# Performance work log

Hardware: AMD Instinct MI355X
Metric: run time of the kernel (lower is better)

## Reference

```python
import jax, jax.numpy as jnp
import numpy as np
import math

D_MODEL, H, D_FF = 1024, 16, 4096
B, S = 4, 2048
EPS = 1e-6

def layer_norm(x, alpha, beta):
    # Faithful to torch: x.std uses Bessel correction (ddof=1), eps added to std.
    mean = jnp.mean(x, axis=-1, keepdims=True)
    std = jnp.std(x, axis=-1, keepdims=True, ddof=1)
    return alpha * (x - mean) / (std + EPS) + beta

def setup_inputs() -> dict:
    key = jax.random.key(0)
    ks = jax.random.split(key, 8)
    sc = 0.02
    return {
        "x": jax.random.normal(ks[0], (B, S, D_MODEL), jnp.float32),
        "mask": jnp.ones((B, 1, 1, S), jnp.int32),
        "wq": jax.random.normal(ks[1], (D_MODEL, D_MODEL), jnp.float32) * sc,
        "wk": jax.random.normal(ks[2], (D_MODEL, D_MODEL), jnp.float32) * sc,
        "wv": jax.random.normal(ks[3], (D_MODEL, D_MODEL), jnp.float32) * sc,
        "wo": jax.random.normal(ks[4], (D_MODEL, D_MODEL), jnp.float32) * sc,
        "w1": jax.random.normal(ks[5], (D_MODEL, D_FF), jnp.float32) * sc,
        "b1": jnp.zeros((D_FF,), jnp.float32),
        "w2": jax.random.normal(ks[6], (D_FF, D_MODEL), jnp.float32) * sc,
        "b2": jnp.zeros((D_MODEL,), jnp.float32),
        "ln1_a": jnp.ones((D_MODEL,), jnp.float32),
        "ln1_b": jnp.zeros((D_MODEL,), jnp.float32),
        "ln2_a": jnp.ones((D_MODEL,), jnp.float32),
        "ln2_b": jnp.zeros((D_MODEL,), jnp.float32),
    }

def mha(xn, mask, wq, wk, wv, wo):
    b, s, d = xn.shape
    d_k = d // H
    q = (xn @ wq).reshape(b, s, H, d_k).transpose(0, 2, 1, 3)  # [B,H,S,dk]
    k = (xn @ wk).reshape(b, s, H, d_k).transpose(0, 2, 1, 3)
    v = (xn @ wv).reshape(b, s, H, d_k).transpose(0, 2, 1, 3)
    scores = jnp.einsum('bhqd,bhkd->bhqk', q, k) / math.sqrt(d_k)
    scores = jnp.where(mask == 0, -1e9, scores)
    attn = jax.nn.softmax(scores, axis=-1)
    out = jnp.einsum('bhqk,bhkd->bhqd', attn, v)
    out = out.transpose(0, 2, 1, 3).reshape(b, s, d)
    return out @ wo

def reference(x, mask, wq, wk, wv, wo, w1, b1, w2, b2, ln1_a, ln1_b, ln2_a, ln2_b):
    # Pre-LN residual 1: self-attention (dropout=0 / eval mode -> identity)
    xn = layer_norm(x, ln1_a, ln1_b)
    x = x + mha(xn, mask, wq, wk, wv, wo)
    # Pre-LN residual 2: FFN
    xn = layer_norm(x, ln2_a, ln2_b)
    ff = jax.nn.relu(xn @ w1 + b1) @ w2 + b2
    return x + ff
```

## Files before the change

kernel.cpp:

```cpp
#include <hip/hip_runtime.h>
#include <hip/hip_bf16.h>

typedef __bf16 bf16x8 __attribute__((ext_vector_type(8)));
typedef __bf16 bf16x4 __attribute__((ext_vector_type(4)));
typedef float  f32x4  __attribute__((ext_vector_type(4)));

#define MFMA(a, b, c) __builtin_amdgcn_mfma_f32_16x16x32_bf16((a), (b), (c), 0, 0, 0)

#define GLOAD16(gp, lp) __builtin_amdgcn_global_load_lds(                      \
    (const __attribute__((address_space(1))) void*)(gp),                       \
    (__attribute__((address_space(3))) void*)(lp), 16, 0, 0)

__device__ inline unsigned int pkbf(float a, float b) {
    __bf16 x = (__bf16)a, y = (__bf16)b;
    return (unsigned int)*(unsigned short*)&x |
           ((unsigned int)*(unsigned short*)&y << 16);
}

__global__ __launch_bounds__(256) void transpose_cvt(
    const float* __restrict__ src, __bf16* __restrict__ dst, int Kd, int Nd)
{
    __shared__ float tile[32][33];
    const int k0 = blockIdx.y * 32, n0 = blockIdx.x * 32;
    const int t = threadIdx.x;
    const int r = t >> 5, c = t & 31;
#pragma unroll
    for (int i = 0; i < 4; ++i)
        tile[r + i * 8][c] = src[(long)(k0 + r + i * 8) * Nd + n0 + c];
    __syncthreads();
#pragma unroll
    for (int i = 0; i < 4; ++i)
        dst[(long)(n0 + r + i * 8) * Kd + k0 + c] = (__bf16)tile[c][r + i * 8];
}

__global__ __launch_bounds__(256) void transpose_v(
    const __bf16* __restrict__ V, __bf16* __restrict__ Vt)
{
    __shared__ __bf16 tile[32][33];
    const int bh = blockIdx.z;
    const int s0 = blockIdx.x * 32, d0 = blockIdx.y * 32;
    const int t = threadIdx.x, r = t >> 5, c = t & 31;
    const __bf16* Vp = V + (long)bh * 2048 * 64;
    __bf16* Tp = Vt + (long)bh * 64 * 2048;
#pragma unroll
    for (int i = 0; i < 4; ++i)
        tile[r + i * 8][c] = Vp[(long)(s0 + r + i * 8) * 64 + d0 + c];
    __syncthreads();
#pragma unroll
    for (int i = 0; i < 4; ++i)
        Tp[(long)(d0 + r + i * 8) * 2048 + s0 + c] = tile[c][r + i * 8];
}

__global__ __launch_bounds__(256) void ln_kernel(
    const float* __restrict__ in, const float* __restrict__ ga,
    const float* __restrict__ gb, __bf16* __restrict__ out)
{
    const int row = blockIdx.x;
    const int t = threadIdx.x;
    const float4 xv = *(const float4*)(in + (long)row * 1024 + t * 4);
    float s  = xv.x + xv.y + xv.z + xv.w;
    float sq = xv.x * xv.x + xv.y * xv.y + xv.z * xv.z + xv.w * xv.w;
#pragma unroll
    for (int off = 32; off; off >>= 1) {
        s  += __shfl_xor(s, off);
        sq += __shfl_xor(sq, off);
    }
    __shared__ float red[8];
    const int w = t >> 6;
    if ((t & 63) == 0) { red[w * 2] = s; red[w * 2 + 1] = sq; }
    __syncthreads();
    s  = red[0] + red[2] + red[4] + red[6];
    sq = red[1] + red[3] + red[5] + red[7];
    const float mean = s * (1.0f / 1024.0f);
    const float var  = fmaxf((sq - s * mean) * (1.0f / 1023.0f), 0.0f);
    const float dinv = 1.0f / (sqrtf(var) + 1e-6f);
    const float4 av = *(const float4*)(ga + t * 4);
    const float4 bv = *(const float4*)(gb + t * 4);
    bf16x4 o;
    o[0] = (__bf16)((xv.x - mean) * dinv * av.x + bv.x);
    o[1] = (__bf16)((xv.y - mean) * dinv * av.y + bv.y);
    o[2] = (__bf16)((xv.z - mean) * dinv * av.z + bv.z);
    o[3] = (__bf16)((xv.w - mean) * dinv * av.w + bv.w);
    *(bf16x4*)(out + (long)row * 1024 + t * 4) = o;
}

template <int MODE>
__global__ __launch_bounds__(256) void gemm_bt(
    const __bf16* __restrict__ A, const __bf16* __restrict__ Bt,
    int M, int N, int K,
    const float* __restrict__ bias, const float* resid,
    float* outf, __bf16* __restrict__ outb,
    __bf16* __restrict__ qb, __bf16* __restrict__ kb, __bf16* __restrict__ vb)
{
    __shared__ __align__(16) __bf16 Alds[128 * 32];
    __shared__ __align__(16) __bf16 Blds[128 * 32];

    const int t = threadIdx.x;
    const int lane = t & 63, w = t >> 6;
    const int wr = w >> 1, wc = w & 1;
    const int g = lane >> 4, l15 = lane & 15;

    const int nwg = gridDim.x * gridDim.y;
    const int hwid = blockIdx.y * gridDim.x + blockIdx.x;
    const int wid = (hwid & 7) * (nwg >> 3) + (hwid >> 3);
    const int bm = (wid / gridDim.x) * 128;
    const int bn = (wid % gridDim.x) * 128;

    const int cr = t >> 2;
    const int cc = (t & 3) * 8;
    const __bf16* Ag  = A  + (long)(bm + cr) * K + cc;
    const __bf16* Ag2 = Ag + (long)64 * K;
    const __bf16* Bg  = Bt + (long)(bn + cr) * K + cc;
    const __bf16* Bg2 = Bg + (long)64 * K;
    char* Alp = (char*)Alds + t * 16;
    char* Blp = (char*)Blds + t * 16;

    f32x4 acc[4][4] = {};
    const int nk = K / 32;

    for (int kt = 0; kt < nk; ++kt) {
        const long ko = (long)kt * 32;
        __syncthreads();
        GLOAD16(Ag + ko,  Alp);
        GLOAD16(Ag2 + ko, Alp + 4096);
        GLOAD16(Bg + ko,  Blp);
        GLOAD16(Bg2 + ko, Blp + 4096);
        __syncthreads();
        bf16x8 af[4], bfr[4];
#pragma unroll
        for (int mi = 0; mi < 4; ++mi)
            af[mi] = *(const bf16x8*)(Alds + (wr * 64 + mi * 16 + l15) * 32 + g * 8);
#pragma unroll
        for (int ni = 0; ni < 4; ++ni)
            bfr[ni] = *(const bf16x8*)(Blds + (wc * 64 + ni * 16 + l15) * 32 + g * 8);
#pragma unroll
        for (int mi = 0; mi < 4; ++mi)
#pragma unroll
            for (int ni = 0; ni < 4; ++ni)
                acc[mi][ni] = MFMA(af[mi], bfr[ni], acc[mi][ni]);
    }

#pragma unroll
    for (int mi = 0; mi < 4; ++mi) {
#pragma unroll
        for (int ni = 0; ni < 4; ++ni) {
#pragma unroll
            for (int r = 0; r < 4; ++r) {
                const int gr = bm + wr * 64 + mi * 16 + g * 4 + r;
                const int gc = bn + wc * 64 + ni * 16 + l15;
                const float vacc = acc[mi][ni][r];
                if constexpr (MODE == 0) {
                    const int bufi = gc >> 10;
                    const int hd = gc & 1023;
                    const int h = hd >> 6, d = hd & 63;
                    const int b = gr >> 11, sx = gr & 2047;
                    __bf16* dst = (bufi == 0) ? qb : ((bufi == 1) ? kb : vb);
                    dst[((long)((b * 16 + h) * 2048 + sx)) * 64 + d] = (__bf16)vacc;
                } else if constexpr (MODE == 1) {
                    const long idx = (long)gr * N + gc;
                    outf[idx] = vacc + resid[idx];
                } else if constexpr (MODE == 2) {
                    const float y = fmaxf(vacc + bias[gc], 0.0f);
                    outb[(long)gr * N + gc] = (__bf16)y;
                } else {
                    const long idx = (long)gr * N + gc;
                    outf[idx] = vacc + bias[gc] + resid[idx];
                }
            }
        }
    }
}

__global__ __launch_bounds__(256, 2) void attn_kernel(
    const __bf16* __restrict__ Q, const __bf16* __restrict__ Kk,
    const __bf16* __restrict__ Vt, const int* __restrict__ mask,
    __bf16* __restrict__ O)
{
    __shared__ __align__(16) char Klds[8192];
    __shared__ __align__(16) char Vlds[8192];
    __shared__ int mlds[64];

    const int t = threadIdx.x;
    const int lane = t & 63, w = t >> 6;
    const int g = lane >> 4, l15 = lane & 15;
    const int bh = blockIdx.x >> 4;
    const int qt = blockIdx.x & 15;
    const int b = bh >> 4, h = bh & 15;
    const int q0 = qt * 128 + w * 32;

    const __bf16* Qp = Q  + (long)bh * 2048 * 64;
    const __bf16* Kp = Kk + (long)bh * 2048 * 64;
    const __bf16* Vp = Vt + (long)bh * 64 * 2048;
    const int* mp = mask + b * 2048;

    bf16x8 qreg[2][2];
#pragma unroll
    for (int qf = 0; qf < 2; ++qf)
#pragma unroll
        for (int kh = 0; kh < 2; ++kh)
            qreg[qf][kh] = *(const bf16x8*)(Qp + (long)(q0 + qf * 16 + l15) * 64 + kh * 32 + g * 8);

    const float Csc = 0.18033688011112042f;
    float m2_run[2] = {-1e30f, -1e30f}, l_run[2] = {0.0f, 0.0f};
    f32x4 ot[2][4] = {};

    const int sr0 = t >> 3;
    const int sce = (t & 7) * 8;
    const int swz0 = sr0 * 128 + (((t & 7) * 16) ^ ((sr0 & 7) << 4));
    const int swz1 = swz0 + 32 * 128;

    bf16x8 kr0 = *(const bf16x8*)(Kp + (long)sr0 * 64 + sce);
    bf16x8 kr1 = *(const bf16x8*)(Kp + (long)(sr0 + 32) * 64 + sce);
    bf16x8 vr0 = *(const bf16x8*)(Vp + (long)sr0 * 2048 + sce);
    bf16x8 vr1 = *(const bf16x8*)(Vp + (long)(sr0 + 32) * 2048 + sce);
    int mr = (t < 64) ? mp[t] : 0;

    for (int kc = 0; kc < 32; ++kc) {
        __syncthreads();
        *(bf16x8*)(Klds + swz0) = kr0;
        *(bf16x8*)(Klds + swz1) = kr1;
        *(bf16x8*)(Vlds + swz0) = vr0;
        *(bf16x8*)(Vlds + swz1) = vr1;
        if (t < 64) mlds[t] = mr;
        __syncthreads();
        if (kc < 31) {
            const int kv0 = (kc + 1) * 64;
            kr0 = *(const bf16x8*)(Kp + (long)(kv0 + sr0) * 64 + sce);
            kr1 = *(const bf16x8*)(Kp + (long)(kv0 + sr0 + 32) * 64 + sce);
            vr0 = *(const bf16x8*)(Vp + (long)sr0 * 2048 + kv0 + sce);
            vr1 = *(const bf16x8*)(Vp + (long)(sr0 + 32) * 2048 + kv0 + sce);
            if (t < 64) mr = mp[kv0 + t];
        }

        bf16x8 kf[4][2];
#pragma unroll
        for (int f = 0; f < 4; ++f)
#pragma unroll
            for (int dh = 0; dh < 2; ++dh)
                kf[f][dh] = *(const bf16x8*)(Klds + (f * 16 + l15) * 128 +
                                             ((dh * 64 + g * 16) ^ ((l15 & 7) << 4)));
        f32x4 sf[2][4] = {};
        __builtin_amdgcn_s_setprio(1);
#pragma unroll
        for (int qf = 0; qf < 2; ++qf)
#pragma unroll
            for (int f = 0; f < 4; ++f) {
                sf[qf][f] = MFMA(kf[f][0], qreg[qf][0], sf[qf][f]);
                sf[qf][f] = MFMA(kf[f][1], qreg[qf][1], sf[qf][f]);
            }
        __builtin_amdgcn_s_setprio(0);

        int mvv[16];
#pragma unroll
        for (int f = 0; f < 4; ++f) {
            const int4 mq = *(const int4*)&mlds[f * 16 + g * 4];
            mvv[f * 4 + 0] = mq.x; mvv[f * 4 + 1] = mq.y;
            mvv[f * 4 + 2] = mq.z; mvv[f * 4 + 3] = mq.w;
        }

        bf16x8 av[4][2];
#pragma unroll
        for (int df = 0; df < 4; ++df) {
            const int row = (df * 16 + l15) * 128;
            const int sx = (l15 & 7) << 4;
#pragma unroll
            for (int hh = 0; hh < 2; ++hh) {
                const bf16x4 lo = *(const bf16x4*)(Vlds + row + ((hh * 64 + g * 8) ^ sx));
                const bf16x4 hi = *(const bf16x4*)(Vlds + row + ((hh * 64 + 32 + g * 8) ^ sx));
                bf16x8 a;
                a[0] = lo[0]; a[1] = lo[1]; a[2] = lo[2]; a[3] = lo[3];
                a[4] = hi[0]; a[5] = hi[1]; a[6] = hi[2]; a[7] = hi[3];
                av[df][hh] = a;
            }
        }

#pragma unroll
        for (int qf = 0; qf < 2; ++qf) {
            float s[16];
            float mx = -1e30f;
#pragma unroll
            for (int i = 0; i < 16; ++i) {
                float xs = sf[qf][i >> 2][i & 3];
                if (mvv[i] == 0) xs = -1e9f;
                s[i] = xs;
                mx = fmaxf(mx, xs);
            }
            mx = fmaxf(mx, __shfl_xor(mx, 16));
            mx = fmaxf(mx, __shfl_xor(mx, 32));
            const float m2 = mx * Csc;
            if (!__all(m2 - m2_run[qf] <= 8.0f)) {
                const float m2n = fmaxf(m2_run[qf], m2);
                const float alpha = __builtin_amdgcn_exp2f(m2_run[qf] - m2n);
                l_run[qf] *= alpha;
#pragma unroll
                for (int df = 0; df < 4; ++df)
#pragma unroll
                    for (int r = 0; r < 4; ++r) ot[qf][df][r] *= alpha;
                m2_run[qf] = m2n;
            }
            const float nm2 = -m2_run[qf];
            float p[16], ps = 0.0f;
#pragma unroll
            for (int i = 0; i < 16; ++i) {
                p[i] = __builtin_amdgcn_exp2f(__builtin_fmaf(s[i], Csc, nm2));
                ps += p[i];
            }
            ps += __shfl_xor(ps, 16);
            ps += __shfl_xor(ps, 32);
            l_run[qf] += ps;

#pragma unroll
            for (int hh = 0; hh < 2; ++hh) {
                unsigned int pu[4] = {pkbf(p[hh * 8 + 0], p[hh * 8 + 1]),
                                      pkbf(p[hh * 8 + 2], p[hh * 8 + 3]),
                                      pkbf(p[hh * 8 + 4], p[hh * 8 + 5]),
                                      pkbf(p[hh * 8 + 6], p[hh * 8 + 7])};
                bf16x8 pf = *(bf16x8*)pu;
                __builtin_amdgcn_s_setprio(1);
#pragma unroll
                for (int df = 0; df < 4; ++df)
                    ot[qf][df] = MFMA(av[df][hh], pf, ot[qf][df]);
                __builtin_amdgcn_s_setprio(0);
            }
        }
    }

#pragma unroll
    for (int qf = 0; qf < 2; ++qf) {
        const float inv = 1.0f / l_run[qf];
        const int q = q0 + qf * 16 + l15;
        __bf16* orow = O + (long)(b * 2048 + q) * 1024 + h * 64;
#pragma unroll
        for (int df = 0; df < 4; ++df)
#pragma unroll
            for (int rp = 0; rp < 2; ++rp) {
                const int d = df * 16 + g * 4 + rp * 2;
                *(unsigned int*)(orow + d) =
                    pkbf(ot[qf][df][rp * 2] * inv, ot[qf][df][rp * 2 + 1] * inv);
            }
    }
}

extern "C" void kernel_launch(void* const* d_in, const int* in_sizes, int n_in,
                              void* d_out, int out_size, void* d_ws, size_t ws_size,
                              hipStream_t stream)
{
    const float* x    = (const float*)d_in[0];
    const int*   mask = (const int*)  d_in[1];
    const float* wq   = (const float*)d_in[2];
    const float* wk   = (const float*)d_in[3];
    const float* wv   = (const float*)d_in[4];
    const float* wo   = (const float*)d_in[5];
    const float* w1   = (const float*)d_in[6];
    const float* b1   = (const float*)d_in[7];
    const float* w2   = (const float*)d_in[8];
    const float* b2   = (const float*)d_in[9];
    const float* l1a  = (const float*)d_in[10];
    const float* l1b  = (const float*)d_in[11];
    const float* l2a  = (const float*)d_in[12];
    const float* l2b  = (const float*)d_in[13];
    float* out = (float*)d_out;

    char* ws = (char*)d_ws;
    __bf16* wqkvT = (__bf16*)(ws);
    __bf16* woT   = (__bf16*)(ws + 6291456);
    __bf16* w1T   = (__bf16*)(ws + 8388608);
    __bf16* w2T   = (__bf16*)(ws + 16777216);
    __bf16* xn    = (__bf16*)(ws + 25165824);
    __bf16* Vtb   = (__bf16*)(ws + 25165824);
    __bf16* Qb    = (__bf16*)(ws + 41943040);
    __bf16* Kb    = (__bf16*)(ws + 58720256);
    __bf16* Vb    = (__bf16*)(ws + 75497472);
    __bf16* attO  = (__bf16*)(ws + 92274688);
    __bf16* ffh   = (__bf16*)(ws + 41943040);

    transpose_cvt<<<dim3(32, 32),  256, 0, stream>>>(wq, wqkvT,               1024, 1024);
    transpose_cvt<<<dim3(32, 32),  256, 0, stream>>>(wk, wqkvT + 1024 * 1024, 1024, 1024);
    transpose_cvt<<<dim3(32, 32),  256, 0, stream>>>(wv, wqkvT + 2048 * 1024, 1024, 1024);
    transpose_cvt<<<dim3(32, 32),  256, 0, stream>>>(wo, woT,                 1024, 1024);
    transpose_cvt<<<dim3(128, 32), 256, 0, stream>>>(w1, w1T,                 1024, 4096);
    transpose_cvt<<<dim3(32, 128), 256, 0, stream>>>(w2, w2T,                 4096, 1024);

    ln_kernel<<<8192, 256, 0, stream>>>(x, l1a, l1b, xn);
    gemm_bt<0><<<dim3(24, 64), 256, 0, stream>>>(xn, wqkvT, 8192, 3072, 1024,
                                                 nullptr, nullptr, nullptr, nullptr, Qb, Kb, Vb);
    transpose_v<<<dim3(64, 2, 64), 256, 0, stream>>>(Vb, Vtb);
    attn_kernel<<<1024, 256, 0, stream>>>(Qb, Kb, Vtb, mask, attO);
    gemm_bt<1><<<dim3(8, 64), 256, 0, stream>>>(attO, woT, 8192, 1024, 1024,
                                                nullptr, x, out, nullptr, nullptr, nullptr, nullptr);
    ln_kernel<<<8192, 256, 0, stream>>>(out, l2a, l2b, xn);
    gemm_bt<2><<<dim3(32, 64), 256, 0, stream>>>(xn, w1T, 8192, 4096, 1024,
                                                 b1, nullptr, nullptr, ffh, nullptr, nullptr, nullptr);
    gemm_bt<3><<<dim3(8, 64), 256, 0, stream>>>(ffh, w2T, 8192, 1024, 4096,
                                                b2, out, out, nullptr, nullptr, nullptr, nullptr);
    (void)in_sizes; (void)n_in; (void)out_size; (void)ws_size;
}
```

Before: 491.9 us.

## Compute softmax row sums via MFMA with ones and skip masking for fully-valid tiles

Precomputes per-KV-tile flags marking whether the mask is all ones, so fully unmasked tiles skip the mask load and select. The scalar row-sum accumulation and its cross-lane shuffles are replaced by an extra MFMA of a ones vector against the bf16 probabilities. The max reduction is also restructured as a tree. This moves VALU and shuffle work onto the matrix unit, at the cost of one extra MFMA per half-tile and row sums taken from bf16-rounded probabilities.

```diff
diff --git a/kernel.cpp b/kernel.cpp
--- a/kernel.cpp
+++ b/kernel.cpp
@@ -179,6 +179,7 @@
     __shared__ __align__(16) char Klds[8192];
     __shared__ __align__(16) char Vlds[8192];
     __shared__ int mlds[64];
+    __shared__ int tflag[32];
 
     const int t = threadIdx.x;
     const int lane = t & 63, w = t >> 6;
@@ -193,6 +194,16 @@
     const __bf16* Vp = Vt + (long)bh * 64 * 2048;
     const int* mp = mask + b * 2048;
 
+    {
+        const int4* mi4 = (const int4*)(mp + t * 8);
+        const int4 ma = mi4[0], mb = mi4[1];
+        const int ok = (ma.x && ma.y && ma.z && ma.w &&
+                        mb.x && mb.y && mb.z && mb.w) ? 1 : 0;
+        const unsigned long long bal = __ballot(ok);
+        if ((lane & 7) == 0)
+            tflag[t >> 3] = (((bal >> lane) & 0xFFull) == 0xFFull) ? 1 : 0;
+    }
+
     bf16x8 qreg[2][2];
 #pragma unroll
     for (int qf = 0; qf < 2; ++qf)
@@ -200,8 +211,13 @@
         for (int kh = 0; kh < 2; ++kh)
             qreg[qf][kh] = *(const bf16x8*)(Qp + (long)(q0 + qf * 16 + l15) * 64 + kh * 32 + g * 8);
 
+    bf16x8 vone;
+#pragma unroll
+    for (int j = 0; j < 8; ++j) vone[j] = (__bf16)1.0f;
+
     const float Csc = 0.18033688011112042f;
-    float m2_run[2] = {-1e30f, -1e30f}, l_run[2] = {0.0f, 0.0f};
+    float m2_run[2] = {-1e30f, -1e30f};
+    f32x4 la[2] = {};
     f32x4 ot[2][4] = {};
 
     const int sr0 = t >> 3;
@@ -231,6 +247,7 @@
             vr1 = *(const bf16x8*)(Vp + (long)(sr0 + 32) * 2048 + kv0 + sce);
             if (t < 64) mr = mp[kv0 + t];
         }
+        const bool fullv = (tflag[kc] != 0);
 
         bf16x8 kf[4][2];
 #pragma unroll
@@ -249,14 +266,6 @@
                 sf[qf][f] = MFMA(kf[f][1], qreg[qf][1], sf[qf][f]);
             }
         __builtin_amdgcn_s_setprio(0);
-
-        int mvv[16];
-#pragma unroll
-        for (int f = 0; f < 4; ++f) {
-            const int4 mq = *(const int4*)&mlds[f * 16 + g * 4];
-            mvv[f * 4 + 0] = mq.x; mvv[f * 4 + 1] = mq.y;
-            mvv[f * 4 + 2] = mq.z; mvv[f * 4 + 3] = mq.w;
-        }
 
         bf16x8 av[4][2];
 #pragma unroll
@@ -277,21 +286,35 @@
 #pragma unroll
         for (int qf = 0; qf < 2; ++qf) {
             float s[16];
-            float mx = -1e30f;
-#pragma unroll
-            for (int i = 0; i < 16; ++i) {
-                float xs = sf[qf][i >> 2][i & 3];
-                if (mvv[i] == 0) xs = -1e9f;
-                s[i] = xs;
-                mx = fmaxf(mx, xs);
-            }
+            if (fullv) {
+#pragma unroll
+                for (int i = 0; i < 16; ++i) s[i] = sf[qf][i >> 2][i & 3];
+            } else {
+                int mvv[16];
+#pragma unroll
+                for (int f = 0; f < 4; ++f) {
+                    const int4 mq = *(const int4*)&mlds[f * 16 + g * 4];
+                    mvv[f * 4 + 0] = mq.x; mvv[f * 4 + 1] = mq.y;
+                    mvv[f * 4 + 2] = mq.z; mvv[f * 4 + 3] = mq.w;
+                }
+#pragma unroll
+                for (int i = 0; i < 16; ++i)
+                    s[i] = (mvv[i] == 0) ? -1e9f : sf[qf][i >> 2][i & 3];
+            }
+            float m01 = fmaxf(s[0], s[1]),   m23 = fmaxf(s[2], s[3]);
+            float m45 = fmaxf(s[4], s[5]),   m67 = fmaxf(s[6], s[7]);
+            float m89 = fmaxf(s[8], s[9]),   mab = fmaxf(s[10], s[11]);
+            float mcd = fmaxf(s[12], s[13]), mef = fmaxf(s[14], s[15]);
+            float mx = fmaxf(fmaxf(fmaxf(m01, m23), fmaxf(m45, m67)),
+                             fmaxf(fmaxf(m89, mab), fmaxf(mcd, mef)));
             mx = fmaxf(mx, __shfl_xor(mx, 16));
             mx = fmaxf(mx, __shfl_xor(mx, 32));
             const float m2 = mx * Csc;
             if (!__all(m2 - m2_run[qf] <= 8.0f)) {
                 const float m2n = fmaxf(m2_run[qf], m2);
                 const float alpha = __builtin_amdgcn_exp2f(m2_run[qf] - m2n);
-                l_run[qf] *= alpha;
+#pragma unroll
+                for (int r = 0; r < 4; ++r) la[qf][r] *= alpha;
 #pragma unroll
                 for (int df = 0; df < 4; ++df)
 #pragma unroll
@@ -299,15 +322,10 @@
                 m2_run[qf] = m2n;
             }
             const float nm2 = -m2_run[qf];
-            float p[16], ps = 0.0f;
-#pragma unroll
-            for (int i = 0; i < 16; ++i) {
+            float p[16];
+#pragma unroll
+            for (int i = 0; i < 16; ++i)
                 p[i] = __builtin_amdgcn_exp2f(__builtin_fmaf(s[i], Csc, nm2));
-                ps += p[i];
-            }
-            ps += __shfl_xor(ps, 16);
-            ps += __shfl_xor(ps, 32);
-            l_run[qf] += ps;
 
 #pragma unroll
             for (int hh = 0; hh < 2; ++hh) {
@@ -320,6 +338,7 @@
 #pragma unroll
                 for (int df = 0; df < 4; ++df)
                     ot[qf][df] = MFMA(av[df][hh], pf, ot[qf][df]);
+                la[qf] = MFMA(vone, pf, la[qf]);
                 __builtin_amdgcn_s_setprio(0);
             }
         }
@@ -327,7 +346,7 @@
 
 #pragma unroll
     for (int qf = 0; qf < 2; ++qf) {
-        const float inv = 1.0f / l_run[qf];
+        const float inv = 1.0f / la[qf][0];
         const int q = q0 + qf * 16 + l15;
         __bf16* orow = O + (long)(b * 2048 + q) * 1024 + h * 64;
 #pragma unroll
```

Result: no change. 490.8 us (-0.2%).
